# Kernel optimization log

Measured on AMD Instinct MI355X. Metric: run time of the kernel, lower is better.

The kernel has to match this reference:

```python
import jax, jax.numpy as jnp
import numpy as np

N, D = 8192, 4096
DIM_K = 4096

def setup_inputs() -> dict:
    key0 = jax.random.key(0)
    k1, k2, k3 = jax.random.split(key0, 3)
    return {
        "query": jax.random.normal(k1, (N, D), dtype=jnp.float32),
        "key": jax.random.normal(k2, (D, N), dtype=jnp.float32),
        "value": jax.random.normal(k3, (N, D), dtype=jnp.float32),
    }

def reference(query, key, value):
    # Faithful to the (buggy) torch module: ELEMENTWISE query * key.T,
    # scale by sqrt(dim_k), elementwise * value, softmax over dim=1
    # (F.softmax's implicit dim for a 2D tensor). The mask branch in the
    # original (`if x:`) cannot execute for multi-element tensors, so it
    # is omitted (mask=None path).
    scale = jnp.sqrt(jnp.float32(DIM_K))
    x = (query * key.T) / scale  # [N, D]
    x = x * value                # [N, D]
    return jax.nn.softmax(x, axis=1)
```

## Files before the change

### kernel.cpp

```cpp
#include <hip/hip_runtime.h>
#include <math.h>


static constexpr int NROW = 8192;
static constexpr int D    = 4096;
static constexpr float SCL = 0.015625f;

__device__ __forceinline__ unsigned short f2bf(float f) {
    unsigned int b = __float_as_uint(f);
    b = (b + 0x7FFFu + ((b >> 16) & 1u)) >> 16;
    return (unsigned short)b;
}
__device__ __forceinline__ float bf2f(unsigned short u) {
    return __uint_as_float(((unsigned int)u) << 16);
}

__global__ __launch_bounds__(256, 2)
void kt_transpose_kernel(const float* __restrict__ K,
                         unsigned short* __restrict__ KT)
{
    __shared__ float lds[64][257];
    const int t  = threadIdx.x;
    const int jt = blockIdx.x & 63;
    const int it = blockIdx.x >> 6;
    const int j0 = jt * 64;
    const int i0 = it * 256;

    const int rr = t >> 6;
    const int i4 = t & 63;
    #pragma unroll
    for (int s = 0; s < 16; ++s) {
        const int jr = s * 4 + rr;
        const float4 v =
            *(const float4*)(K + (size_t)(j0 + jr) * NROW + i0 + 4 * i4);
        *(float4*)&lds[jr][4 * i4] = v;
    }
    __syncthreads();

    const int j4 = t & 15;
    const int ir = t >> 4;
    #pragma unroll
    for (int sw = 0; sw < 16; ++sw) {
        const int il = sw * 16 + ir;
        ushort4 w;
        w.x = f2bf(lds[4 * j4 + 0][il]);
        w.y = f2bf(lds[4 * j4 + 1][il]);
        w.z = f2bf(lds[4 * j4 + 2][il]);
        w.w = f2bf(lds[4 * j4 + 3][il]);
        *(ushort4*)(KT + (size_t)(i0 + il) * D + j0 + 4 * j4) = w;
    }
}

__global__ __launch_bounds__(256, 4)
void sdp_stream_kernel(const float* __restrict__ Q,
                       const unsigned short* __restrict__ KT,
                       const float* __restrict__ V,
                       float* __restrict__ O)
{
    const int tid  = threadIdx.x;
    const int wv   = tid >> 6;
    const int lane = tid & 63;
    const int r    = blockIdx.x * 4 + wv;

    const float*          qrow = Q  + (size_t)r * D;
    const unsigned short* krow = KT + (size_t)r * D;
    const float*          vrow = V  + (size_t)r * D;
    float*                orow = O  + (size_t)r * D;
    const int c0 = 4 * lane;

    float4  qA = *(const float4*)(qrow + 0 * 256 + c0);
    ushort4 kA = *(const ushort4*)(krow + 0 * 256 + c0);
    float4  vA = *(const float4*)(vrow + 0 * 256 + c0);
    float4  qB = *(const float4*)(qrow + 1 * 256 + c0);
    ushort4 kB = *(const ushort4*)(krow + 1 * 256 + c0);
    float4  vB = *(const float4*)(vrow + 1 * 256 + c0);
    float4  qC = *(const float4*)(qrow + 2 * 256 + c0);
    ushort4 kC = *(const ushort4*)(krow + 2 * 256 + c0);
    float4  vC = *(const float4*)(vrow + 2 * 256 + c0);
    float4  qD = *(const float4*)(qrow + 3 * 256 + c0);
    ushort4 kD = *(const ushort4*)(krow + 3 * 256 + c0);
    float4  vD = *(const float4*)(vrow + 3 * 256 + c0);

    ushort4 e0, e1, e2, e3, e4, e5, e6, e7,
            e8, e9, e10, e11, e12, e13, e14, e15;
    float s = 0.0f;

#define BODY(t, ET, QS, KS, VS)                                               \
    {                                                                         \
        const float4 qc = QS; const ushort4 kc = KS; const float4 vc = VS;    \
        if ((t) + 4 < 16) {                                                   \
            QS = *(const float4*)(qrow + ((t) + 4) * 256 + c0);               \
            KS = *(const ushort4*)(krow + ((t) + 4) * 256 + c0);              \
            VS = *(const float4*)(vrow + ((t) + 4) * 256 + c0);               \
        }                                                                     \
        const float ex = __expf(((qc.x * bf2f(kc.x)) * SCL) * vc.x);          \
        const float ey = __expf(((qc.y * bf2f(kc.y)) * SCL) * vc.y);          \
        const float ez = __expf(((qc.z * bf2f(kc.z)) * SCL) * vc.z);          \
        const float ew = __expf(((qc.w * bf2f(kc.w)) * SCL) * vc.w);          \
        s += ((ex + ey) + (ez + ew));                                         \
        ET.x = f2bf(ex); ET.y = f2bf(ey); ET.z = f2bf(ez); ET.w = f2bf(ew);   \
        __builtin_amdgcn_sched_barrier(0);                                    \
    }

    BODY(0,  e0,  qA, kA, vA)
    BODY(1,  e1,  qB, kB, vB)
    BODY(2,  e2,  qC, kC, vC)
    BODY(3,  e3,  qD, kD, vD)
    BODY(4,  e4,  qA, kA, vA)
    BODY(5,  e5,  qB, kB, vB)
    BODY(6,  e6,  qC, kC, vC)
    BODY(7,  e7,  qD, kD, vD)
    BODY(8,  e8,  qA, kA, vA)
    BODY(9,  e9,  qB, kB, vB)
    BODY(10, e10, qC, kC, vC)
    BODY(11, e11, qD, kD, vD)
    BODY(12, e12, qA, kA, vA)
    BODY(13, e13, qB, kB, vB)
    BODY(14, e14, qC, kC, vC)
    BODY(15, e15, qD, kD, vD)
#undef BODY

    #pragma unroll
    for (int i = 1; i < 64; i <<= 1)
        s += __shfl_xor(s, i, 64);
    const float inv = 1.0f / s;

#define WRITE_TILE(t, ET)                                                     \
    {                                                                         \
        float4 xx;                                                            \
        xx.x = bf2f(ET.x) * inv;                                              \
        xx.y = bf2f(ET.y) * inv;                                              \
        xx.z = bf2f(ET.z) * inv;                                              \
        xx.w = bf2f(ET.w) * inv;                                              \
        *(float4*)(orow + (size_t)(t) * 256 + c0) = xx;                       \
    }

    WRITE_TILE(0,  e0)  WRITE_TILE(1,  e1)  WRITE_TILE(2,  e2)  WRITE_TILE(3,  e3)
    WRITE_TILE(4,  e4)  WRITE_TILE(5,  e5)  WRITE_TILE(6,  e6)  WRITE_TILE(7,  e7)
    WRITE_TILE(8,  e8)  WRITE_TILE(9,  e9)  WRITE_TILE(10, e10) WRITE_TILE(11, e11)
    WRITE_TILE(12, e12) WRITE_TILE(13, e13) WRITE_TILE(14, e14) WRITE_TILE(15, e15)
#undef WRITE_TILE
}

extern "C" void kernel_launch(void* const* d_in, const int* in_sizes, int n_in,
                              void* d_out, int out_size, void* d_ws, size_t ws_size,
                              hipStream_t stream) {
    const float* Q = (const float*)d_in[0];
    const float* K = (const float*)d_in[1];
    const float* V = (const float*)d_in[2];
    float* O = (float*)d_out;

    unsigned short* KT = (unsigned short*)d_ws;
    kt_transpose_kernel<<<dim3(64 * 32), dim3(256), 0, stream>>>(K, KT);
    sdp_stream_kernel<<<dim3(NROW / 4), dim3(256), 0, stream>>>(Q, KT, V, O);
}
```

Measured before the change: 140.3 us.

## Split each softmax row across two waves and shrink transpose tiles

```diff
diff --git a/kernel.cpp b/kernel.cpp
--- a/kernel.cpp
+++ b/kernel.cpp
@@ -15,22 +15,22 @@
     return __uint_as_float(((unsigned int)u) << 16);
 }
 
-__global__ __launch_bounds__(256, 2)
+__global__ __launch_bounds__(256, 4)
 void kt_transpose_kernel(const float* __restrict__ K,
                          unsigned short* __restrict__ KT)
 {
-    __shared__ float lds[64][257];
+    __shared__ float lds[64][129];
     const int t  = threadIdx.x;
     const int jt = blockIdx.x & 63;
     const int it = blockIdx.x >> 6;
     const int j0 = jt * 64;
-    const int i0 = it * 256;
+    const int i0 = it * 128;
 
-    const int rr = t >> 6;
-    const int i4 = t & 63;
+    const int i4 = t & 31;
+    const int jb = t >> 5;
     #pragma unroll
-    for (int s = 0; s < 16; ++s) {
-        const int jr = s * 4 + rr;
+    for (int s = 0; s < 8; ++s) {
+        const int jr = s * 8 + jb;
         const float4 v =
             *(const float4*)(K + (size_t)(j0 + jr) * NROW + i0 + 4 * i4);
         *(float4*)&lds[jr][4 * i4] = v;
@@ -38,10 +38,10 @@
     __syncthreads();
 
     const int j4 = t & 15;
-    const int ir = t >> 4;
+    const int ib = t >> 4;
     #pragma unroll
-    for (int sw = 0; sw < 16; ++sw) {
-        const int il = sw * 16 + ir;
+    for (int sw = 0; sw < 8; ++sw) {
+        const int il = sw * 16 + ib;
         ushort4 w;
         w.x = f2bf(lds[4 * j4 + 0][il]);
         w.y = f2bf(lds[4 * j4 + 1][il]);
@@ -51,21 +51,24 @@
     }
 }
 
-__global__ __launch_bounds__(256, 4)
+__global__ __launch_bounds__(256, 6)
 void sdp_stream_kernel(const float* __restrict__ Q,
                        const unsigned short* __restrict__ KT,
                        const float* __restrict__ V,
                        float* __restrict__ O)
 {
+    __shared__ float ssum[4];
+
     const int tid  = threadIdx.x;
     const int wv   = tid >> 6;
     const int lane = tid & 63;
-    const int r    = blockIdx.x * 4 + wv;
+    const int r    = blockIdx.x * 2 + (wv >> 1);
+    const int hbase = (wv & 1) * 2048;
 
-    const float*          qrow = Q  + (size_t)r * D;
-    const unsigned short* krow = KT + (size_t)r * D;
-    const float*          vrow = V  + (size_t)r * D;
-    float*                orow = O  + (size_t)r * D;
+    const float*          qrow = Q  + (size_t)r * D + hbase;
+    const unsigned short* krow = KT + (size_t)r * D + hbase;
+    const float*          vrow = V  + (size_t)r * D + hbase;
+    float*                orow = O  + (size_t)r * D + hbase;
     const int c0 = 4 * lane;
 
     float4  qA = *(const float4*)(qrow + 0 * 256 + c0);
@@ -81,14 +84,13 @@
     ushort4 kD = *(const ushort4*)(krow + 3 * 256 + c0);
     float4  vD = *(const float4*)(vrow + 3 * 256 + c0);
 
-    ushort4 e0, e1, e2, e3, e4, e5, e6, e7,
-            e8, e9, e10, e11, e12, e13, e14, e15;
+    ushort4 e0, e1, e2, e3, e4, e5, e6, e7;
     float s = 0.0f;
 
 #define BODY(t, ET, QS, KS, VS)                                               \
     {                                                                         \
         const float4 qc = QS; const ushort4 kc = KS; const float4 vc = VS;    \
-        if ((t) + 4 < 16) {                                                   \
+        if ((t) + 4 < 8) {                                                    \
             QS = *(const float4*)(qrow + ((t) + 4) * 256 + c0);               \
             KS = *(const ushort4*)(krow + ((t) + 4) * 256 + c0);              \
             VS = *(const float4*)(vrow + ((t) + 4) * 256 + c0);               \
@@ -102,28 +104,22 @@
         __builtin_amdgcn_sched_barrier(0);                                    \
     }
 
-    BODY(0,  e0,  qA, kA, vA)
-    BODY(1,  e1,  qB, kB, vB)
-    BODY(2,  e2,  qC, kC, vC)
-    BODY(3,  e3,  qD, kD, vD)
-    BODY(4,  e4,  qA, kA, vA)
-    BODY(5,  e5,  qB, kB, vB)
-    BODY(6,  e6,  qC, kC, vC)
-    BODY(7,  e7,  qD, kD, vD)
-    BODY(8,  e8,  qA, kA, vA)
-    BODY(9,  e9,  qB, kB, vB)
-    BODY(10, e10, qC, kC, vC)
-    BODY(11, e11, qD, kD, vD)
-    BODY(12, e12, qA, kA, vA)
-    BODY(13, e13, qB, kB, vB)
-    BODY(14, e14, qC, kC, vC)
-    BODY(15, e15, qD, kD, vD)
+    BODY(0, e0, qA, kA, vA)
+    BODY(1, e1, qB, kB, vB)
+    BODY(2, e2, qC, kC, vC)
+    BODY(3, e3, qD, kD, vD)
+    BODY(4, e4, qA, kA, vA)
+    BODY(5, e5, qB, kB, vB)
+    BODY(6, e6, qC, kC, vC)
+    BODY(7, e7, qD, kD, vD)
 #undef BODY
 
     #pragma unroll
     for (int i = 1; i < 64; i <<= 1)
         s += __shfl_xor(s, i, 64);
-    const float inv = 1.0f / s;
+    if (lane == 0) ssum[wv] = s;
+    __syncthreads();
+    const float inv = 1.0f / (ssum[wv] + ssum[wv ^ 1]);
 
 #define WRITE_TILE(t, ET)                                                     \
     {                                                                         \
@@ -135,10 +131,8 @@
         *(float4*)(orow + (size_t)(t) * 256 + c0) = xx;                       \
     }
 
-    WRITE_TILE(0,  e0)  WRITE_TILE(1,  e1)  WRITE_TILE(2,  e2)  WRITE_TILE(3,  e3)
-    WRITE_TILE(4,  e4)  WRITE_TILE(5,  e5)  WRITE_TILE(6,  e6)  WRITE_TILE(7,  e7)
-    WRITE_TILE(8,  e8)  WRITE_TILE(9,  e9)  WRITE_TILE(10, e10) WRITE_TILE(11, e11)
-    WRITE_TILE(12, e12) WRITE_TILE(13, e13) WRITE_TILE(14, e14) WRITE_TILE(15, e15)
+    WRITE_TILE(0, e0)  WRITE_TILE(1, e1)  WRITE_TILE(2, e2)  WRITE_TILE(3, e3)
+    WRITE_TILE(4, e4)  WRITE_TILE(5, e5)  WRITE_TILE(6, e6)  WRITE_TILE(7, e7)
 #undef WRITE_TILE
 }
 
@@ -151,6 +145,6 @@
     float* O = (float*)d_out;
 
     unsigned short* KT = (unsigned short*)d_ws;
-    kt_transpose_kernel<<<dim3(64 * 32), dim3(256), 0, stream>>>(K, KT);
-    sdp_stream_kernel<<<dim3(NROW / 4), dim3(256), 0, stream>>>(Q, KT, V, O);
+    kt_transpose_kernel<<<dim3(64 * 64), dim3(256), 0, stream>>>(K, KT);
+    sdp_stream_kernel<<<dim3(NROW / 2), dim3(256), 0, stream>>>(Q, KT, V, O);
 }
```

New measurement: 133.1 us. 1.05x faster.
